# Optimization experiments

Measured on AMD Instinct MI355X. Metric: run time of the kernel, lower is better.

The kernel has to match this reference:

```python
import jax, jax.numpy as jnp
import numpy as np

B, T, K, QD = 8, 256, 128, 128  # t-1 = 255 neighbors per agent

def setup_inputs() -> dict:
    key = jax.random.key(0)
    ks = jax.random.split(key, 8)
    q_x = jax.random.normal(ks[0], (B, T, QD), dtype=jnp.float32)
    kv_x = jax.random.normal(ks[1], (B, T, T - 1, K), dtype=jnp.float32)
    # weights stored as (in, out) so y = x @ W  (== torch Linear with weight W.T)
    Wk = jax.random.normal(ks[2], (K, K), dtype=jnp.float32) / np.sqrt(K)
    Wq = jax.random.normal(ks[3], (QD, K), dtype=jnp.float32) / np.sqrt(QD)
    Wv = jax.random.normal(ks[4], (K, K), dtype=jnp.float32) / np.sqrt(K)
    bias = jax.random.uniform(ks[5], (K,), dtype=jnp.float32, minval=-0.1, maxval=0.1)
    score_w = jax.random.normal(ks[6], (K,), dtype=jnp.float32) / np.sqrt(K)
    score_b = jax.random.normal(ks[7], (), dtype=jnp.float32) * 0.01
    return {"q_x": q_x, "kv_x": kv_x, "Wk": Wk, "Wq": Wq, "Wv": Wv,
            "bias": bias, "score_w": score_w, "score_b": score_b}

def reference(q_x, kv_x, Wk, Wq, Wv, bias, score_w, score_b):
    # keys: (b, t, t-1, k); queries: (b, t, 1, k)
    keys = jnp.einsum('btnk,kj->btnj', kv_x, Wk)
    queries = jnp.einsum('btq,qj->btj', q_x, Wq)[:, :, None, :]
    # additive score: tanh(broadcast add) projected to scalar per neighbor
    score = jnp.einsum('btnk,k->btn', jnp.tanh(keys + queries + bias), score_w) + score_b
    w = jax.nn.softmax(score, axis=-1)  # (b, t, t-1)
    values = jnp.einsum('btnk,kj->btnj', kv_x, Wv)
    x = jnp.einsum('btn,btnk->btk', w, values)  # weighted sum over neighbors
    return x
```

## Files before the change

### kernel.cpp

```cpp
#include <hip/hip_runtime.h>
#include <hip/hip_bf16.h>

#define NNEI 255
#define KD 128

typedef __bf16 bf16_t;
typedef __bf16 bf16x8 __attribute__((ext_vector_type(8)));
typedef __bf16 bf16x4 __attribute__((ext_vector_type(4)));
typedef __bf16 bf16x2 __attribute__((ext_vector_type(2)));
typedef float f32x4 __attribute__((ext_vector_type(4)));

__device__ __forceinline__ float fast_tanh(float x) {
    float e = __expf(2.f * x);
    return 1.f - 2.f / (e + 1.f);
}

__global__ __launch_bounds__(256, 3)
void raa_kernel(const float* __restrict__ q_x, const float* __restrict__ kv_x,
                const float* __restrict__ Wk, const float* __restrict__ Wq,
                const float* __restrict__ Wv, const float* __restrict__ bias,
                const float* __restrict__ score_w, float* __restrict__ out) {
    __shared__ __align__(16) unsigned char sWkT[128 * 256];
    __shared__ __align__(16) unsigned char sKV[64 * 256];
    __shared__ float sQ[128];
    __shared__ float sQB[128];
    __shared__ float sM[4];
    __shared__ float sL[4];
    __shared__ __align__(16) float sAcc[4][128];
    __shared__ float sXP[128];

    const int bt = blockIdx.x;
    const int tid = threadIdx.x;
    const int lane = tid & 63;
    const int w = tid >> 6;

    if (tid < 128) sQ[tid] = q_x[bt * 128 + tid];

    {
        int j = tid >> 1;
        int i0 = (tid & 1) * 64;
        for (int s8 = 0; s8 < 8; ++s8) {
            bf16x8 pk;
            #pragma unroll
            for (int u = 0; u < 8; ++u)
                pk[u] = (bf16_t)Wk[(i0 + s8 * 8 + u) * 128 + j];
            unsigned off = (unsigned)(j * 256 + (i0 + s8 * 8) * 2) ^ ((unsigned)(j & 7) << 4);
            *(bf16x8*)(sWkT + off) = pk;
        }
    }
    __syncthreads();

    if (tid < 128) {
        float a = bias[tid];
        for (int i = 0; i < 128; ++i)
            a = fmaf(sQ[i], Wq[i * 128 + tid], a);
        sQB[tid] = a;
    }
    __syncthreads();

    const int r0 = lane & 15;
    const int g4 = lane >> 4;
    float qb_r[8], sw_r[8];
    #pragma unroll
    for (int jt = 0; jt < 8; ++jt) {
        qb_r[jt] = sQB[jt * 16 + r0];
        sw_r[jt] = score_w[jt * 16 + r0];
    }

    const float4* kv4 = (const float4*)(kv_x + (size_t)bt * NNEI * KD);

    float m_run = -3e38f, l_run = 0.f, acc0 = 0.f, acc1 = 0.f;

    for (int c = 0; c < 4; ++c) {
        #pragma unroll
        for (int q = 0; q < 8; ++q) {
            int idx = tid + 256 * q;
            int g = c * 2048 + idx;
            float4 v = make_float4(0.f, 0.f, 0.f, 0.f);
            if (g < NNEI * 32) v = kv4[g];
            bf16x4 pk;
            pk[0] = (bf16_t)v.x; pk[1] = (bf16_t)v.y;
            pk[2] = (bf16_t)v.z; pk[3] = (bf16_t)v.w;
            unsigned a = (unsigned)idx * 8;
            unsigned row = a >> 8;
            unsigned off = a ^ ((row & 7) << 4);
            *(bf16x4*)(sKV + off) = pk;
        }
        __syncthreads();

        f32x4 Ck[8];
        #pragma unroll
        for (int jt = 0; jt < 8; ++jt) Ck[jt] = (f32x4){0.f, 0.f, 0.f, 0.f};
        const int rowA = w * 16 + r0;
        const unsigned swzA = ((unsigned)(rowA & 7) << 4);
        #pragma unroll
        for (int ks = 0; ks < 4; ++ks) {
            bf16x8 af = *(const bf16x8*)(sKV +
                (((unsigned)(rowA * 256 + ks * 64 + g4 * 16)) ^ swzA));
            #pragma unroll
            for (int jt = 0; jt < 8; ++jt) {
                int nr = jt * 16 + r0;
                bf16x8 bfr = *(const bf16x8*)(sWkT +
                    (((unsigned)(nr * 256 + ks * 64 + g4 * 16)) ^ ((unsigned)(nr & 7) << 4)));
                Ck[jt] = __builtin_amdgcn_mfma_f32_16x16x32_bf16(af, bfr, Ck[jt], 0, 0, 0);
            }
        }

        float part[4] = {0.f, 0.f, 0.f, 0.f};
        #pragma unroll
        for (int jt = 0; jt < 8; ++jt) {
            #pragma unroll
            for (int reg = 0; reg < 4; ++reg) {
                float x = Ck[jt][reg] + qb_r[jt];
                part[reg] = fmaf(fast_tanh(x), sw_r[jt], part[reg]);
            }
        }
        #pragma unroll
        for (int off = 1; off < 16; off <<= 1) {
            #pragma unroll
            for (int reg = 0; reg < 4; ++reg)
                part[reg] += __shfl_xor(part[reg], off);
        }
        float sc4[4];
        #pragma unroll
        for (int reg = 0; reg < 4; ++reg) {
            int n = c * 64 + w * 16 + g4 * 4 + reg;
            sc4[reg] = (n < NNEI) ? part[reg] : -1e30f;
        }
        float cm = fmaxf(fmaxf(sc4[0], sc4[1]), fmaxf(sc4[2], sc4[3]));
        cm = fmaxf(cm, __shfl_xor(cm, 16));
        cm = fmaxf(cm, __shfl_xor(cm, 32));
        float mn = fmaxf(m_run, cm);
        float scale = __expf(m_run - mn);
        float p[4];
        #pragma unroll
        for (int reg = 0; reg < 4; ++reg) p[reg] = __expf(sc4[reg] - mn);
        float ps = p[0] + p[1] + p[2] + p[3];
        ps += __shfl_xor(ps, 16);
        ps += __shfl_xor(ps, 32);
        l_run = l_run * scale + ps;
        m_run = mn;
        acc0 *= scale; acc1 *= scale;
        #pragma unroll
        for (int r = 0; r < 16; ++r) {
            float pb = __shfl(p[r & 3], (r >> 2) * 16);
            int rowK = w * 16 + r;
            unsigned off = ((unsigned)(rowK * 256 + lane * 4)) ^ ((unsigned)(rowK & 7) << 4);
            bf16x2 kvv = *(const bf16x2*)(sKV + off);
            acc0 = fmaf(pb, (float)kvv[0], acc0);
            acc1 = fmaf(pb, (float)kvv[1], acc1);
        }
        __syncthreads();
    }

    if (lane == 0) { sM[w] = m_run; sL[w] = l_run; }
    sAcc[w][2 * lane]     = acc0;
    sAcc[w][2 * lane + 1] = acc1;
    __syncthreads();

    if (tid < 128) {
        float M4 = fmaxf(fmaxf(sM[0], sM[1]), fmaxf(sM[2], sM[3]));
        float f0 = __expf(sM[0] - M4), f1 = __expf(sM[1] - M4),
              f2 = __expf(sM[2] - M4), f3 = __expf(sM[3] - M4);
        float L = f0 * sL[0] + f1 * sL[1] + f2 * sL[2] + f3 * sL[3];
        float xp = f0 * sAcc[0][tid] + f1 * sAcc[1][tid]
                 + f2 * sAcc[2][tid] + f3 * sAcc[3][tid];
        sXP[tid] = xp / L;
    }
    __syncthreads();

    if (tid < 128) {
        float o = 0.f;
        for (int j = 0; j < 128; ++j)
            o = fmaf(sXP[j], Wv[j * 128 + tid], o);
        out[(size_t)bt * 128 + tid] = o;
    }
}

extern "C" void kernel_launch(void* const* d_in, const int* in_sizes, int n_in,
                              void* d_out, int out_size, void* d_ws, size_t ws_size,
                              hipStream_t stream) {
    const float* q_x     = (const float*)d_in[0];
    const float* kv_x    = (const float*)d_in[1];
    const float* Wk      = (const float*)d_in[2];
    const float* Wq      = (const float*)d_in[3];
    const float* Wv      = (const float*)d_in[4];
    const float* bias    = (const float*)d_in[5];
    const float* score_w = (const float*)d_in[6];
    float* out = (float*)d_out;

    raa_kernel<<<dim3(2048), dim3(256), 0, stream>>>(
        q_x, kv_x, Wk, Wq, Wv, bias, score_w, out);
}
```

Baseline: 108.4 us.

## Load kv rows directly into MFMA fragments, drop kv LDS staging

Each wave now loads its own 64 kv rows from global memory straight into registers, converts them to bf16 MFMA A fragments, and reuses those same registers for the weighted value sum. This removes the shared kv staging buffer and the per-chunk barriers. Wk's k dimension is permuted so each lane's contiguous 32-float row slice matches the MFMA K ordering. The Wq and Wv matvecs are split across all 256 threads, and launch bounds drop to 2 blocks per CU to make room for the larger register footprint (32 accumulators plus fragments), which lowers occupancy.

```diff
diff --git a/kernel.cpp b/kernel.cpp
--- a/kernel.cpp
+++ b/kernel.cpp
@@ -2,12 +2,9 @@
 #include <hip/hip_bf16.h>
 
 #define NNEI 255
-#define KD 128
 
 typedef __bf16 bf16_t;
 typedef __bf16 bf16x8 __attribute__((ext_vector_type(8)));
-typedef __bf16 bf16x4 __attribute__((ext_vector_type(4)));
-typedef __bf16 bf16x2 __attribute__((ext_vector_type(2)));
 typedef float f32x4 __attribute__((ext_vector_type(4)));
 
 __device__ __forceinline__ float fast_tanh(float x) {
@@ -15,17 +12,16 @@
     return 1.f - 2.f / (e + 1.f);
 }
 
-__global__ __launch_bounds__(256, 3)
+__global__ __launch_bounds__(256, 2)
 void raa_kernel(const float* __restrict__ q_x, const float* __restrict__ kv_x,
                 const float* __restrict__ Wk, const float* __restrict__ Wq,
                 const float* __restrict__ Wv, const float* __restrict__ bias,
                 const float* __restrict__ score_w, float* __restrict__ out) {
     __shared__ __align__(16) unsigned char sWkT[128 * 256];
-    __shared__ __align__(16) unsigned char sKV[64 * 256];
     __shared__ float sQ[128];
+    __shared__ float sQBp[2][128];
     __shared__ float sQB[128];
-    __shared__ float sM[4];
-    __shared__ float sL[4];
+    __shared__ float sM[4], sL[4];
     __shared__ __align__(16) float sAcc[4][128];
     __shared__ float sXP[128];
 
@@ -33,33 +29,38 @@
     const int tid = threadIdx.x;
     const int lane = tid & 63;
     const int w = tid >> 6;
-
-    if (tid < 128) sQ[tid] = q_x[bt * 128 + tid];
-
-    {
-        int j = tid >> 1;
-        int i0 = (tid & 1) * 64;
-        for (int s8 = 0; s8 < 8; ++s8) {
-            bf16x8 pk;
-            #pragma unroll
-            for (int u = 0; u < 8; ++u)
-                pk[u] = (bf16_t)Wk[(i0 + s8 * 8 + u) * 128 + j];
-            unsigned off = (unsigned)(j * 256 + (i0 + s8 * 8) * 2) ^ ((unsigned)(j & 7) << 4);
-            *(bf16x8*)(sWkT + off) = pk;
-        }
-    }
-    __syncthreads();
-
-    if (tid < 128) {
-        float a = bias[tid];
-        for (int i = 0; i < 128; ++i)
-            a = fmaf(sQ[i], Wq[i * 128 + tid], a);
-        sQB[tid] = a;
-    }
-    __syncthreads();
-
     const int r0 = lane & 15;
     const int g4 = lane >> 4;
+
+    if (tid < 128) sQ[tid] = q_x[bt * 128 + tid];
+
+    {
+        int j = tid >> 1, i0 = (tid & 1) * 64;
+        #pragma unroll
+        for (int s8 = 0; s8 < 8; ++s8) {
+            int kk0 = i0 + s8 * 8;
+            int ks = kk0 >> 5, gs = (kk0 >> 3) & 3;
+            bf16x8 pk;
+            #pragma unroll
+            for (int u = 0; u < 8; ++u)
+                pk[u] = (bf16_t)Wk[(gs * 32 + ks * 8 + u) * 128 + j];
+            unsigned off = (unsigned)(j * 256 + kk0 * 2) ^ ((unsigned)(j & 7) << 4);
+            *(bf16x8*)(sWkT + off) = pk;
+        }
+    }
+    __syncthreads();
+
+    {
+        int j = tid & 127, h = tid >> 7;
+        float a = 0.f;
+        for (int i = h * 64; i < h * 64 + 64; ++i)
+            a = fmaf(sQ[i], Wq[i * 128 + j], a);
+        sQBp[h][j] = a;
+    }
+    __syncthreads();
+    if (tid < 128) sQB[tid] = sQBp[0][tid] + sQBp[1][tid] + bias[tid];
+    __syncthreads();
+
     float qb_r[8], sw_r[8];
     #pragma unroll
     for (int jt = 0; jt < 8; ++jt) {
@@ -67,101 +68,143 @@
         sw_r[jt] = score_w[jt * 16 + r0];
     }
 
-    const float4* kv4 = (const float4*)(kv_x + (size_t)bt * NNEI * KD);
-
-    float m_run = -3e38f, l_run = 0.f, acc0 = 0.f, acc1 = 0.f;
-
-    for (int c = 0; c < 4; ++c) {
-        #pragma unroll
-        for (int q = 0; q < 8; ++q) {
-            int idx = tid + 256 * q;
-            int g = c * 2048 + idx;
-            float4 v = make_float4(0.f, 0.f, 0.f, 0.f);
-            if (g < NNEI * 32) v = kv4[g];
-            bf16x4 pk;
-            pk[0] = (bf16_t)v.x; pk[1] = (bf16_t)v.y;
-            pk[2] = (bf16_t)v.z; pk[3] = (bf16_t)v.w;
-            unsigned a = (unsigned)idx * 8;
-            unsigned row = a >> 8;
-            unsigned off = a ^ ((row & 7) << 4);
-            *(bf16x4*)(sKV + off) = pk;
-        }
-        __syncthreads();
-
-        f32x4 Ck[8];
-        #pragma unroll
-        for (int jt = 0; jt < 8; ++jt) Ck[jt] = (f32x4){0.f, 0.f, 0.f, 0.f};
-        const int rowA = w * 16 + r0;
-        const unsigned swzA = ((unsigned)(rowA & 7) << 4);
+    const float4* kv4 = (const float4*)(kv_x) + (size_t)bt * (NNEI * 32);
+
+    float m_run = -3e38f, l_run = 0.f;
+    float acc[32];
+    #pragma unroll
+    for (int u = 0; u < 32; ++u) acc[u] = 0.f;
+
+    #pragma unroll
+    for (int p = 0; p < 2; ++p) {
+        const int rbase = w * 64 + p * 32;
+        float4 v[2][8];
+        #pragma unroll
+        for (int t = 0; t < 2; ++t) {
+            int row = rbase + t * 16 + r0;
+            int rowc = row < NNEI ? row : NNEI - 1;
+            const float4* src = kv4 + rowc * 32 + g4 * 8;
+            #pragma unroll
+            for (int i = 0; i < 8; ++i) v[t][i] = src[i];
+        }
+        bf16x8 afr[2][4];
+        #pragma unroll
+        for (int t = 0; t < 2; ++t) {
+            #pragma unroll
+            for (int ks = 0; ks < 4; ++ks) {
+                bf16x8 f;
+                f[0] = (bf16_t)v[t][2 * ks].x;     f[1] = (bf16_t)v[t][2 * ks].y;
+                f[2] = (bf16_t)v[t][2 * ks].z;     f[3] = (bf16_t)v[t][2 * ks].w;
+                f[4] = (bf16_t)v[t][2 * ks + 1].x; f[5] = (bf16_t)v[t][2 * ks + 1].y;
+                f[6] = (bf16_t)v[t][2 * ks + 1].z; f[7] = (bf16_t)v[t][2 * ks + 1].w;
+                afr[t][ks] = f;
+            }
+        }
+        f32x4 Ck[2][8];
+        #pragma unroll
+        for (int t = 0; t < 2; ++t)
+            #pragma unroll
+            for (int jt = 0; jt < 8; ++jt) Ck[t][jt] = (f32x4){0.f, 0.f, 0.f, 0.f};
         #pragma unroll
         for (int ks = 0; ks < 4; ++ks) {
-            bf16x8 af = *(const bf16x8*)(sKV +
-                (((unsigned)(rowA * 256 + ks * 64 + g4 * 16)) ^ swzA));
             #pragma unroll
             for (int jt = 0; jt < 8; ++jt) {
-                int nr = jt * 16 + r0;
+                int n = jt * 16 + r0;
                 bf16x8 bfr = *(const bf16x8*)(sWkT +
-                    (((unsigned)(nr * 256 + ks * 64 + g4 * 16)) ^ ((unsigned)(nr & 7) << 4)));
-                Ck[jt] = __builtin_amdgcn_mfma_f32_16x16x32_bf16(af, bfr, Ck[jt], 0, 0, 0);
-            }
-        }
-
-        float part[4] = {0.f, 0.f, 0.f, 0.f};
+                    (((unsigned)(n * 256 + ks * 64 + g4 * 16)) ^ ((unsigned)(n & 7) << 4)));
+                Ck[0][jt] = __builtin_amdgcn_mfma_f32_16x16x32_bf16(afr[0][ks], bfr, Ck[0][jt], 0, 0, 0);
+                Ck[1][jt] = __builtin_amdgcn_mfma_f32_16x16x32_bf16(afr[1][ks], bfr, Ck[1][jt], 0, 0, 0);
+            }
+        }
+        float part[2][4];
+        #pragma unroll
+        for (int t = 0; t < 2; ++t)
+            #pragma unroll
+            for (int reg = 0; reg < 4; ++reg) part[t][reg] = 0.f;
         #pragma unroll
         for (int jt = 0; jt < 8; ++jt) {
             #pragma unroll
+            for (int t = 0; t < 2; ++t) {
+                #pragma unroll
+                for (int reg = 0; reg < 4; ++reg) {
+                    float x = Ck[t][jt][reg] + qb_r[jt];
+                    part[t][reg] = fmaf(fast_tanh(x), sw_r[jt], part[t][reg]);
+                }
+            }
+        }
+        #pragma unroll
+        for (int off = 1; off < 16; off <<= 1) {
+            #pragma unroll
+            for (int t = 0; t < 2; ++t)
+                #pragma unroll
+                for (int reg = 0; reg < 4; ++reg)
+                    part[t][reg] += __shfl_xor(part[t][reg], off);
+        }
+        #pragma unroll
+        for (int t = 0; t < 2; ++t) {
+            #pragma unroll
             for (int reg = 0; reg < 4; ++reg) {
-                float x = Ck[jt][reg] + qb_r[jt];
-                part[reg] = fmaf(fast_tanh(x), sw_r[jt], part[reg]);
-            }
-        }
-        #pragma unroll
-        for (int off = 1; off < 16; off <<= 1) {
-            #pragma unroll
-            for (int reg = 0; reg < 4; ++reg)
-                part[reg] += __shfl_xor(part[reg], off);
-        }
-        float sc4[4];
-        #pragma unroll
-        for (int reg = 0; reg < 4; ++reg) {
-            int n = c * 64 + w * 16 + g4 * 4 + reg;
-            sc4[reg] = (n < NNEI) ? part[reg] : -1e30f;
-        }
-        float cm = fmaxf(fmaxf(sc4[0], sc4[1]), fmaxf(sc4[2], sc4[3]));
+                int n = rbase + t * 16 + g4 * 4 + reg;
+                if (n >= NNEI) part[t][reg] = -1e30f;
+            }
+        }
+        float cm = part[0][0];
+        #pragma unroll
+        for (int t = 0; t < 2; ++t)
+            #pragma unroll
+            for (int reg = 0; reg < 4; ++reg) cm = fmaxf(cm, part[t][reg]);
         cm = fmaxf(cm, __shfl_xor(cm, 16));
         cm = fmaxf(cm, __shfl_xor(cm, 32));
         float mn = fmaxf(m_run, cm);
         float scale = __expf(m_run - mn);
-        float p[4];
-        #pragma unroll
-        for (int reg = 0; reg < 4; ++reg) p[reg] = __expf(sc4[reg] - mn);
-        float ps = p[0] + p[1] + p[2] + p[3];
+        float pv[2][4];
+        float ps = 0.f;
+        #pragma unroll
+        for (int t = 0; t < 2; ++t)
+            #pragma unroll
+            for (int reg = 0; reg < 4; ++reg) {
+                pv[t][reg] = __expf(part[t][reg] - mn);
+                ps += pv[t][reg];
+            }
         ps += __shfl_xor(ps, 16);
         ps += __shfl_xor(ps, 32);
         l_run = l_run * scale + ps;
         m_run = mn;
-        acc0 *= scale; acc1 *= scale;
-        #pragma unroll
-        for (int r = 0; r < 16; ++r) {
-            float pb = __shfl(p[r & 3], (r >> 2) * 16);
-            int rowK = w * 16 + r;
-            unsigned off = ((unsigned)(rowK * 256 + lane * 4)) ^ ((unsigned)(rowK & 7) << 4);
-            bf16x2 kvv = *(const bf16x2*)(sKV + off);
-            acc0 = fmaf(pb, (float)kvv[0], acc0);
-            acc1 = fmaf(pb, (float)kvv[1], acc1);
-        }
-        __syncthreads();
-    }
-
+        #pragma unroll
+        for (int u = 0; u < 32; ++u) acc[u] *= scale;
+        #pragma unroll
+        for (int t = 0; t < 2; ++t) {
+            int src = (r0 >> 2) * 16;
+            float a0 = __shfl(pv[t][0], src), a1 = __shfl(pv[t][1], src);
+            float a2 = __shfl(pv[t][2], src), a3 = __shfl(pv[t][3], src);
+            float pr = (r0 & 2) ? ((r0 & 1) ? a3 : a2) : ((r0 & 1) ? a1 : a0);
+            #pragma unroll
+            for (int ks = 0; ks < 4; ++ks)
+                #pragma unroll
+                for (int u = 0; u < 8; ++u)
+                    acc[ks * 8 + u] = fmaf(pr, (float)afr[t][ks][u], acc[ks * 8 + u]);
+        }
+    }
+
+    #pragma unroll
+    for (int off = 1; off < 16; off <<= 1)
+        #pragma unroll
+        for (int u = 0; u < 32; ++u)
+            acc[u] += __shfl_xor(acc[u], off);
+    if (r0 == 0) {
+        #pragma unroll
+        for (int i = 0; i < 8; ++i) {
+            float4 o = make_float4(acc[4 * i], acc[4 * i + 1], acc[4 * i + 2], acc[4 * i + 3]);
+            *(float4*)&sAcc[w][g4 * 32 + 4 * i] = o;
+        }
+    }
     if (lane == 0) { sM[w] = m_run; sL[w] = l_run; }
-    sAcc[w][2 * lane]     = acc0;
-    sAcc[w][2 * lane + 1] = acc1;
     __syncthreads();
 
     if (tid < 128) {
         float M4 = fmaxf(fmaxf(sM[0], sM[1]), fmaxf(sM[2], sM[3]));
-        float f0 = __expf(sM[0] - M4), f1 = __expf(sM[1] - M4),
-              f2 = __expf(sM[2] - M4), f3 = __expf(sM[3] - M4);
+        float f0 = __expf(sM[0] - M4), f1 = __expf(sM[1] - M4);
+        float f2 = __expf(sM[2] - M4), f3 = __expf(sM[3] - M4);
         float L = f0 * sL[0] + f1 * sL[1] + f2 * sL[2] + f3 * sL[3];
         float xp = f0 * sAcc[0][tid] + f1 * sAcc[1][tid]
                  + f2 * sAcc[2][tid] + f3 * sAcc[3][tid];
@@ -169,12 +212,15 @@
     }
     __syncthreads();
 
-    if (tid < 128) {
+    {
+        int j = tid & 127, h = tid >> 7;
         float o = 0.f;
-        for (int j = 0; j < 128; ++j)
-            o = fmaf(sXP[j], Wv[j * 128 + tid], o);
-        out[(size_t)bt * 128 + tid] = o;
-    }
+        for (int i = h * 64; i < h * 64 + 64; ++i)
+            o = fmaf(sXP[i], Wv[i * 128 + j], o);
+        sQBp[h][j] = o;
+    }
+    __syncthreads();
+    if (tid < 128) out[(size_t)bt * 128 + tid] = sQBp[0][tid] + sQBp[1][tid];
 }
 
 extern "C" void kernel_launch(void* const* d_in, const int* in_sizes, int n_in,
```

Measured after the change: 295.8 us. 173% more time.

## Reuse MFMA A-fragments in registers for the softmax-weighted KV accumulation

Applied to the files above, without the earlier changes.

Hoists the four bf16x8 A-fragments of the KV tile into registers and reuses them for the weighted sum over neighbors. Each lane now keeps 32 partial accumulators for its row's columns and scales them by its own row's probability, instead of doing 16 strided LDS reads and shuffles per chunk. A cross-lane shuffle reduction over the 16 rows runs once at the end. This removes LDS traffic from the inner loop, but adds 32 accumulator registers and a larger final reduction, which could hurt occupancy under launch_bounds(256,3).

```diff
diff --git a/kernel.cpp b/kernel.cpp
--- a/kernel.cpp
+++ b/kernel.cpp
@@ -7,7 +7,6 @@
 typedef __bf16 bf16_t;
 typedef __bf16 bf16x8 __attribute__((ext_vector_type(8)));
 typedef __bf16 bf16x4 __attribute__((ext_vector_type(4)));
-typedef __bf16 bf16x2 __attribute__((ext_vector_type(2)));
 typedef float f32x4 __attribute__((ext_vector_type(4)));
 
 __device__ __forceinline__ float fast_tanh(float x) {
@@ -69,7 +68,13 @@
 
     const float4* kv4 = (const float4*)(kv_x + (size_t)bt * NNEI * KD);
 
-    float m_run = -3e38f, l_run = 0.f, acc0 = 0.f, acc1 = 0.f;
+    float m_run = -3e38f, l_run = 0.f;
+    float acc[32];
+    #pragma unroll
+    for (int u = 0; u < 32; ++u) acc[u] = 0.f;
+
+    const int rowA = w * 16 + r0;
+    const unsigned swzA = ((unsigned)(rowA & 7) << 4);
 
     for (int c = 0; c < 4; ++c) {
         #pragma unroll
@@ -88,21 +93,23 @@
         }
         __syncthreads();
 
+        bf16x8 afr[4];
+        #pragma unroll
+        for (int ks = 0; ks < 4; ++ks)
+            afr[ks] = *(const bf16x8*)(sKV +
+                (((unsigned)(rowA * 256 + ks * 64 + g4 * 16)) ^ swzA));
+
         f32x4 Ck[8];
         #pragma unroll
         for (int jt = 0; jt < 8; ++jt) Ck[jt] = (f32x4){0.f, 0.f, 0.f, 0.f};
-        const int rowA = w * 16 + r0;
-        const unsigned swzA = ((unsigned)(rowA & 7) << 4);
         #pragma unroll
         for (int ks = 0; ks < 4; ++ks) {
-            bf16x8 af = *(const bf16x8*)(sKV +
-                (((unsigned)(rowA * 256 + ks * 64 + g4 * 16)) ^ swzA));
             #pragma unroll
             for (int jt = 0; jt < 8; ++jt) {
                 int nr = jt * 16 + r0;
                 bf16x8 bfr = *(const bf16x8*)(sWkT +
                     (((unsigned)(nr * 256 + ks * 64 + g4 * 16)) ^ ((unsigned)(nr & 7) << 4)));
-                Ck[jt] = __builtin_amdgcn_mfma_f32_16x16x32_bf16(af, bfr, Ck[jt], 0, 0, 0);
+                Ck[jt] = __builtin_amdgcn_mfma_f32_16x16x32_bf16(afr[ks], bfr, Ck[jt], 0, 0, 0);
             }
         }
 
@@ -140,22 +147,37 @@
         ps += __shfl_xor(ps, 32);
         l_run = l_run * scale + ps;
         m_run = mn;
-        acc0 *= scale; acc1 *= scale;
-        #pragma unroll
-        for (int r = 0; r < 16; ++r) {
-            float pb = __shfl(p[r & 3], (r >> 2) * 16);
-            int rowK = w * 16 + r;
-            unsigned off = ((unsigned)(rowK * 256 + lane * 4)) ^ ((unsigned)(rowK & 7) << 4);
-            bf16x2 kvv = *(const bf16x2*)(sKV + off);
-            acc0 = fmaf(pb, (float)kvv[0], acc0);
-            acc1 = fmaf(pb, (float)kvv[1], acc1);
+        #pragma unroll
+        for (int u = 0; u < 32; ++u) acc[u] *= scale;
+        {
+            int src = (r0 >> 2) * 16;
+            float a0 = __shfl(p[0], src), a1 = __shfl(p[1], src);
+            float a2 = __shfl(p[2], src), a3 = __shfl(p[3], src);
+            float pr = (r0 & 2) ? ((r0 & 1) ? a3 : a2) : ((r0 & 1) ? a1 : a0);
+            #pragma unroll
+            for (int ks = 0; ks < 4; ++ks)
+                #pragma unroll
+                for (int u = 0; u < 8; ++u)
+                    acc[ks * 8 + u] = fmaf(pr, (float)afr[ks][u], acc[ks * 8 + u]);
         }
         __syncthreads();
     }
 
+    #pragma unroll
+    for (int off = 1; off < 16; off <<= 1)
+        #pragma unroll
+        for (int u = 0; u < 32; ++u)
+            acc[u] += __shfl_xor(acc[u], off);
+    if (r0 == 0) {
+        #pragma unroll
+        for (int ks = 0; ks < 4; ++ks) {
+            *(float4*)&sAcc[w][ks * 32 + g4 * 8] =
+                make_float4(acc[ks * 8 + 0], acc[ks * 8 + 1], acc[ks * 8 + 2], acc[ks * 8 + 3]);
+            *(float4*)&sAcc[w][ks * 32 + g4 * 8 + 4] =
+                make_float4(acc[ks * 8 + 4], acc[ks * 8 + 5], acc[ks * 8 + 6], acc[ks * 8 + 7]);
+        }
+    }
     if (lane == 0) { sM[w] = m_run; sL[w] = l_run; }
-    sAcc[w][2 * lane]     = acc0;
-    sAcc[w][2 * lane + 1] = acc1;
     __syncthreads();
 
     if (tid < 128) {
```

Measured after the change: 126.7 us. 1.17x slower.
